# Kernel tuning notes

Measured on AMD Instinct MI355X. Metric: run time of the kernel, lower is better.

## Reference

```python
import math
import jax, jax.numpy as jnp
import numpy as np


def _procrustes_R(H):
    # H: [B, 3, 3]. Rotation R = V @ U^T with reflection fix (det(R) >= 0),
    # matching torch.svd convention (v = V, not V^T).
    u, s, vh = jnp.linalg.svd(H)
    v = jnp.swapaxes(vh, -1, -2)                       # [B,3,3]
    r = jnp.einsum('bij,bkj->bik', v, u)               # V @ U^T
    det = jnp.linalg.det(r)                            # [B]
    sign = jnp.where(det < 0, -1.0, 1.0)               # flip last column of V (reflect = diag(1,1,-1))
    flip = jnp.stack([jnp.ones_like(sign), jnp.ones_like(sign), sign], axis=-1)[:, None, :]
    v = v * flip
    return jnp.einsum('bij,bkj->bik', v, u)


def setup_inputs() -> dict:
    key = jax.random.key(0)
    k1, k2, k3, k4 = jax.random.split(key, 4)
    B, D, N, M = 8, 512, 2048, 2048
    return {
        'src_embedding': jax.random.normal(k1, (B, D, N), dtype=jnp.float32),
        'tgt_embedding': jax.random.normal(k2, (B, D, M), dtype=jnp.float32),
        'src': jax.random.normal(k3, (B, 3, N), dtype=jnp.float32),
        'tgt': jax.random.normal(k4, (B, 3, M), dtype=jnp.float32),
    }


def reference(src_embedding, tgt_embedding, src, tgt):
    d_k = src_embedding.shape[1]
    # attention correspondence: scores[b,n,m]
    scores = jnp.einsum('bdn,bdm->bnm', src_embedding, tgt_embedding) / math.sqrt(d_k)
    scores = jax.nn.softmax(scores, axis=2)
    # soft correspondence of src points in tgt: [B,3,N]
    src_corr = jnp.einsum('bdm,bnm->bdn', tgt, scores)
    src_mean = src.mean(axis=2, keepdims=True)          # [B,3,1]
    src_centered = src - src_mean
    src_corr_centered = src_corr - src_corr.mean(axis=2, keepdims=True)
    H = jnp.einsum('bin,bjn->bij', src_centered, src_corr_centered)  # [B,3,3]
    R = _procrustes_R(H)
    t = jnp.einsum('bij,bjk->bik', -R, src_mean) + tgt.mean(axis=2, keepdims=True)
    return R, t.reshape(src.shape[0], 3)
```

## Files before the change

### kernel.cpp

```cpp
#include <hip/hip_runtime.h>
#include <hip/hip_bf16.h>

#define BQ 8
#define DIM 512
#define NN 2048
#define MM 2048
#define MSPLIT 16

typedef __attribute__((ext_vector_type(8))) short short8;
typedef __attribute__((ext_vector_type(8))) unsigned short ushort8;
typedef __attribute__((ext_vector_type(4))) float floatx4;

#define GLOAD_LDS(gp, lp) \
    __builtin_amdgcn_global_load_lds( \
        (const __attribute__((address_space(1))) void*)(gp), \
        (__attribute__((address_space(3))) void*)(lp), 16, 0, 0)


static __device__ __forceinline__ unsigned short f2bf(float x) {
    __hip_bfloat16 h = __float2bfloat16(x);
    return *(unsigned short*)&h;
}

__global__ __launch_bounds__(256) void transpose_cast_kernel(
    const float* __restrict__ src_emb,
    const float* __restrict__ tgt_emb,
    __hip_bfloat16* __restrict__ Abf,
    __hip_bfloat16* __restrict__ Bbf)
{
    const int n0 = blockIdx.x * 64;
    const int d0 = blockIdx.y * 64;
    const int b  = blockIdx.z & 7;
    const int which = blockIdx.z >> 3;

    const float* in = (which == 0 ? src_emb : tgt_emb) + (size_t)b * DIM * NN;
    __hip_bfloat16* out = (which == 0 ? Abf : Bbf) + (size_t)b * NN * DIM;

    __shared__ float tl[64][65];

    const int t = threadIdx.x;

    {
        const int u = t & 15;
        const int r = t >> 4;
        #pragma unroll
        for (int rr = r; rr < 64; rr += 16) {
            float4 v = *(const float4*)&in[(size_t)(d0 + rr) * NN + n0 + u * 4];
            tl[rr][u * 4 + 0] = v.x;
            tl[rr][u * 4 + 1] = v.y;
            tl[rr][u * 4 + 2] = v.z;
            tl[rr][u * 4 + 3] = v.w;
        }
    }
    __syncthreads();

    {
        const int u = t & 7;
        const int r = t >> 3;
        #pragma unroll
        for (int rn = r; rn < 64; rn += 32) {
            ushort8 o;
            #pragma unroll
            for (int j = 0; j < 8; j++)
                o[j] = f2bf(tl[u * 8 + j][rn]);
            *(ushort8*)&out[(size_t)(n0 + rn) * DIM + d0 + u * 8] = o;
        }
    }
}

__global__ __launch_bounds__(256, 2) void attn_mfma_kernel(
    const __hip_bfloat16* __restrict__ Abf,
    const __hip_bfloat16* __restrict__ Bbf,
    const float* __restrict__ tgt,
    float* __restrict__ part)
{
    const int nt = blockIdx.x;
    const int qt = blockIdx.y;
    const int b  = blockIdx.z;
    const int t  = threadIdx.x;
    const int wave = t >> 6;
    const int lane = t & 63;
    const int lm   = lane & 15;
    const int quad = lane >> 4;
    const int wn   = wave * 32;

    __shared__ short As[128 * 64];
    __shared__ short Bs[128 * 64];

    const __hip_bfloat16* Abase = Abf + ((size_t)(b * NN + nt * 128)) * DIM;
    const int m0 = qt * 128;
    const __hip_bfloat16* Bbase = Bbf + ((size_t)(b * MM + m0)) * DIM;
    const float* Tb = tgt + (size_t)b * 3 * MM;

    const float SCALE = 0.044194173824159216f * 1.4426950408889634f;

    const int r8 = lane >> 3;
    const int c8 = lane & 7;
    const int cc = c8 ^ r8;
    const __hip_bfloat16* gA = Abase + (size_t)(wn + r8) * DIM + cc * 8;
    const __hip_bfloat16* gB = Bbase + (size_t)(wn + r8) * DIM + cc * 8;
    short* lA = &As[wn * 64];
    short* lB = &Bs[wn * 64];

    floatx4 acc[2][8];
    #pragma unroll
    for (int i = 0; i < 2; i++)
        #pragma unroll
        for (int j = 0; j < 8; j++)
            acc[i][j] = (floatx4){0.f, 0.f, 0.f, 0.f};

    #pragma unroll
    for (int kt = 0; kt < 8; kt++) {
        #pragma unroll
        for (int i = 0; i < 4; i++) {
            GLOAD_LDS(gA + kt * 64 + (size_t)i * 8 * DIM, lA + i * 512);
            GLOAD_LDS(gB + kt * 64 + (size_t)i * 8 * DIM, lB + i * 512);
        }
        __syncthreads();

        #pragma unroll
        for (int ks = 0; ks < 2; ks++) {
            const int pc = (((ks * 4 + quad) ^ (lane & 7)) * 8);
            short8 af0 = *(const short8*)&As[(wn +      lm) * 64 + pc];
            short8 af1 = *(const short8*)&As[(wn + 16 + lm) * 64 + pc];
            #pragma unroll
            for (int j = 0; j < 8; j++) {
                short8 bf = *(const short8*)&Bs[(j * 16 + lm) * 64 + pc];
                acc[0][j] = __builtin_amdgcn_mfma_f32_16x16x32_bf16(af0, bf, acc[0][j], 0, 0, 0);
                acc[1][j] = __builtin_amdgcn_mfma_f32_16x16x32_bf16(af1, bf, acc[1][j], 0, 0, 0);
            }
        }
        __syncthreads();
    }

    float v0[8], v1[8], v2[8];
    #pragma unroll
    for (int j = 0; j < 8; j++) {
        int vc = m0 + j * 16 + lm;
        v0[j] = Tb[vc];
        v1[j] = Tb[MM + vc];
        v2[j] = Tb[2 * MM + vc];
    }

    const size_t slot = (size_t)(b * MSPLIT + qt) * NN;
    #pragma unroll
    for (int i = 0; i < 2; i++) {
        float l4[4] = {0,0,0,0};
        float o0[4] = {0,0,0,0};
        float o1[4] = {0,0,0,0};
        float o2[4] = {0,0,0,0};
        #pragma unroll
        for (int j = 0; j < 8; j++) {
            #pragma unroll
            for (int r = 0; r < 4; r++) {
                float e = __builtin_amdgcn_exp2f(acc[i][j][r] * SCALE);
                l4[r] += e;
                o0[r] += e * v0[j];
                o1[r] += e * v1[j];
                o2[r] += e * v2[j];
            }
        }
        #pragma unroll
        for (int m = 1; m <= 8; m <<= 1) {
            #pragma unroll
            for (int r = 0; r < 4; r++) {
                l4[r] += __shfl_xor(l4[r], m);
                o0[r] += __shfl_xor(o0[r], m);
                o1[r] += __shfl_xor(o1[r], m);
                o2[r] += __shfl_xor(o2[r], m);
            }
        }
        if (lm == 0) {
            #pragma unroll
            for (int r = 0; r < 4; r++) {
                int n = nt * 128 + wn + i * 16 + quad * 4 + r;
                ((float4*)part)[slot + n] = make_float4(l4[r], o0[r], o1[r], o2[r]);
            }
        }
    }
}

__global__ __launch_bounds__(128) void reduce1_kernel(
    const float* __restrict__ part,
    const float* __restrict__ src,
    const float* __restrict__ tgt,
    float* __restrict__ red)
{
    const int chunk = blockIdx.x;
    const int b     = blockIdx.y;
    const int t     = threadIdx.x;
    const int n     = chunk * 128 + t;

    const float4* w4 = (const float4*)part;
    const float* S = src + (size_t)b * 3 * NN;
    const float* T = tgt + (size_t)b * 3 * MM;

    float l = 0.f, y0 = 0.f, y1 = 0.f, y2 = 0.f;
    #pragma unroll
    for (int q = 0; q < 16; q++) {
        float4 p = w4[(size_t)(b * 16 + q) * NN + n];
        l += p.x; y0 += p.y; y1 += p.z; y2 += p.w;
    }
    float inv = 1.0f / l;
    float c0 = y0 * inv, c1 = y1 * inv, c2 = y2 * inv;
    float s0 = S[n], s1 = S[NN + n], s2 = S[2 * NN + n];

    float vals[18];
    vals[0] = s0;  vals[1] = s1;  vals[2] = s2;
    vals[3] = c0;  vals[4] = c1;  vals[5] = c2;
    vals[6] = T[n]; vals[7] = T[MM + n]; vals[8] = T[2 * MM + n];
    vals[9]  = s0 * c0; vals[10] = s0 * c1; vals[11] = s0 * c2;
    vals[12] = s1 * c0; vals[13] = s1 * c1; vals[14] = s1 * c2;
    vals[15] = s2 * c0; vals[16] = s2 * c1; vals[17] = s2 * c2;

    #pragma unroll
    for (int m = 1; m <= 32; m <<= 1)
        #pragma unroll
        for (int c = 0; c < 18; c++)
            vals[c] += __shfl_xor(vals[c], m);

    __shared__ float w0[18];
    if (t == 64)
        #pragma unroll
        for (int c = 0; c < 18; c++) w0[c] = vals[c];
    __syncthreads();
    if (t == 0)
        #pragma unroll
        for (int c = 0; c < 18; c++)
            red[(size_t)(b * 16 + chunk) * 18 + c] = vals[c] + w0[c];
}

__global__ __launch_bounds__(64) void procrustes_kernel(
    const float* __restrict__ red,
    float* __restrict__ out)
{
    const int b = blockIdx.x;
    const int t = threadIdx.x;

    __shared__ float res[18];
    if (t < 18) {
        float a = 0.f;
        #pragma unroll
        for (int q = 0; q < 16; q++)
            a += red[(size_t)(b * 16 + q) * 18 + t];
        res[t] = a;
    }
    __syncthreads();

    if (t == 0) {
        const float invN = 1.0f / (float)NN;
        float mus[3], muc[3], mut[3], H[3][3];
        for (int i = 0; i < 3; i++) {
            mus[i] = res[i] * invN;
            muc[i] = res[3 + i] * invN;
            mut[i] = res[6 + i] * invN;
        }
        for (int i = 0; i < 3; i++)
            for (int j = 0; j < 3; j++)
                H[i][j] = res[9 + i * 3 + j] - (float)NN * mus[i] * muc[j];

        float A[3][3];
        for (int i = 0; i < 3; i++)
            for (int j = 0; j < 3; j++)
                A[i][j] = H[0][i] * H[0][j] + H[1][i] * H[1][j] + H[2][i] * H[2][j];

        float V[3][3] = {{1,0,0},{0,1,0},{0,0,1}};
        for (int sweep = 0; sweep < 6; sweep++) {
            for (int pi = 0; pi < 3; pi++) {
                int p = (pi < 2) ? 0 : 1;
                int q = (pi == 0) ? 1 : 2;
                float apq = A[p][q];
                if (fabsf(apq) < 1e-30f) continue;
                float tau = (A[q][q] - A[p][p]) / (2.0f * apq);
                float tt = (tau >= 0.0f) ? 1.0f / (tau + sqrtf(1.0f + tau * tau))
                                         : -1.0f / (-tau + sqrtf(1.0f + tau * tau));
                float c = 1.0f / sqrtf(1.0f + tt * tt);
                float s = tt * c;
                for (int k = 0; k < 3; k++) {
                    float akp = A[k][p], akq = A[k][q];
                    A[k][p] = c * akp - s * akq;
                    A[k][q] = s * akp + c * akq;
                }
                for (int k = 0; k < 3; k++) {
                    float apk = A[p][k], aqk = A[q][k];
                    A[p][k] = c * apk - s * aqk;
                    A[q][k] = s * apk + c * aqk;
                }
                for (int k = 0; k < 3; k++) {
                    float vkp = V[k][p], vkq = V[k][q];
                    V[k][p] = c * vkp - s * vkq;
                    V[k][q] = s * vkp + c * vkq;
                }
            }
        }

        float lam[3] = {A[0][0], A[1][1], A[2][2]};
        int idx[3] = {0, 1, 2};
        for (int a = 0; a < 2; a++)
            for (int bb = 0; bb < 2 - a; bb++)
                if (lam[idx[bb]] < lam[idx[bb + 1]]) { int tmp = idx[bb]; idx[bb] = idx[bb + 1]; idx[bb + 1] = tmp; }

        float Vc[3][3], U[3][3];
        for (int c = 0; c < 3; c++) {
            float sv = sqrtf(fmaxf(lam[idx[c]], 0.0f));
            float isv = 1.0f / fmaxf(sv, 1e-20f);
            for (int r = 0; r < 3; r++) {
                Vc[r][c] = V[r][idx[c]];
                U[r][c] = (H[r][0] * V[0][idx[c]] + H[r][1] * V[1][idx[c]] + H[r][2] * V[2][idx[c]]) * isv;
            }
        }

        {
            float nrm = rsqrtf(U[0][0]*U[0][0] + U[1][0]*U[1][0] + U[2][0]*U[2][0]);
            for (int r = 0; r < 3; r++) U[r][0] *= nrm;
            float d01 = U[0][0]*U[0][1] + U[1][0]*U[1][1] + U[2][0]*U[2][1];
            for (int r = 0; r < 3; r++) U[r][1] -= d01 * U[r][0];
            nrm = rsqrtf(U[0][1]*U[0][1] + U[1][1]*U[1][1] + U[2][1]*U[2][1]);
            for (int r = 0; r < 3; r++) U[r][1] *= nrm;
            float d02 = U[0][0]*U[0][2] + U[1][0]*U[1][2] + U[2][0]*U[2][2];
            float d12 = U[0][1]*U[0][2] + U[1][1]*U[1][2] + U[2][1]*U[2][2];
            for (int r = 0; r < 3; r++) U[r][2] -= d02 * U[r][0] + d12 * U[r][1];
            nrm = rsqrtf(U[0][2]*U[0][2] + U[1][2]*U[1][2] + U[2][2]*U[2][2]);
            for (int r = 0; r < 3; r++) U[r][2] *= nrm;
        }

        float det = H[0][0]*(H[1][1]*H[2][2] - H[1][2]*H[2][1])
                  - H[0][1]*(H[1][0]*H[2][2] - H[1][2]*H[2][0])
                  + H[0][2]*(H[1][0]*H[2][1] - H[1][1]*H[2][0]);
        float sgn = (det < 0.0f) ? -1.0f : 1.0f;

        float R[3][3];
        for (int i = 0; i < 3; i++)
            for (int j = 0; j < 3; j++)
                R[i][j] = Vc[i][0]*U[j][0] + Vc[i][1]*U[j][1] + sgn * Vc[i][2]*U[j][2];

        for (int i = 0; i < 3; i++)
            for (int j = 0; j < 3; j++)
                out[b * 9 + i * 3 + j] = R[i][j];
        for (int i = 0; i < 3; i++)
            out[BQ * 9 + b * 3 + i] = mut[i] - (R[i][0]*mus[0] + R[i][1]*mus[1] + R[i][2]*mus[2]);
    }
}

extern "C" void kernel_launch(void* const* d_in, const int* in_sizes, int n_in,
                              void* d_out, int out_size, void* d_ws, size_t ws_size,
                              hipStream_t stream) {
    const float* src_emb = (const float*)d_in[0];
    const float* tgt_emb = (const float*)d_in[1];
    const float* src     = (const float*)d_in[2];
    const float* tgt     = (const float*)d_in[3];
    float* out = (float*)d_out;

    float* part = (float*)d_ws;
    __hip_bfloat16* Abf = (__hip_bfloat16*)((char*)d_ws + (4 << 20));
    __hip_bfloat16* Bbf = (__hip_bfloat16*)((char*)d_ws + (20 << 20));
    float* red = (float*)((char*)d_ws + (36 << 20));

    dim3 gridT(NN / 64, DIM / 64, 2 * BQ);
    transpose_cast_kernel<<<gridT, 256, 0, stream>>>(src_emb, tgt_emb, Abf, Bbf);

    dim3 gridA(NN / 128, MSPLIT, BQ);
    attn_mfma_kernel<<<gridA, 256, 0, stream>>>(Abf, Bbf, tgt, part);

    dim3 gridR(16, BQ);
    reduce1_kernel<<<gridR, 128, 0, stream>>>(part, src, tgt, red);

    procrustes_kernel<<<BQ, 64, 0, stream>>>(red, out);
}
```

Before: 172.0 us.

## Use 2x2 wave tiling in attention MFMA kernel with LDS partial combine

Result: slower. 176.2 us (+2.5%).

```diff
diff --git a/kernel.cpp b/kernel.cpp
--- a/kernel.cpp
+++ b/kernel.cpp
@@ -82,10 +82,13 @@
     const int lane = t & 63;
     const int lm   = lane & 15;
     const int quad = lane >> 4;
-    const int wn   = wave * 32;
+    const int nh = wave >> 1;
+    const int mh = wave & 1;
+    const int wn = wave * 32;
 
     __shared__ short As[128 * 64];
     __shared__ short Bs[128 * 64];
+    __shared__ float4 sc4[2][128];
 
     const __hip_bfloat16* Abase = Abf + ((size_t)(b * NN + nt * 128)) * DIM;
     const int m0 = qt * 128;
@@ -102,11 +105,11 @@
     short* lA = &As[wn * 64];
     short* lB = &Bs[wn * 64];
 
-    floatx4 acc[2][8];
-    #pragma unroll
-    for (int i = 0; i < 2; i++)
-        #pragma unroll
-        for (int j = 0; j < 8; j++)
+    floatx4 acc[4][4];
+    #pragma unroll
+    for (int i = 0; i < 4; i++)
+        #pragma unroll
+        for (int j = 0; j < 4; j++)
             acc[i][j] = (floatx4){0.f, 0.f, 0.f, 0.f};
 
     #pragma unroll
@@ -120,37 +123,41 @@
 
         #pragma unroll
         for (int ks = 0; ks < 2; ks++) {
-            const int pc = (((ks * 4 + quad) ^ (lane & 7)) * 8);
-            short8 af0 = *(const short8*)&As[(wn +      lm) * 64 + pc];
-            short8 af1 = *(const short8*)&As[(wn + 16 + lm) * 64 + pc];
-            #pragma unroll
-            for (int j = 0; j < 8; j++) {
-                short8 bf = *(const short8*)&Bs[(j * 16 + lm) * 64 + pc];
-                acc[0][j] = __builtin_amdgcn_mfma_f32_16x16x32_bf16(af0, bf, acc[0][j], 0, 0, 0);
-                acc[1][j] = __builtin_amdgcn_mfma_f32_16x16x32_bf16(af1, bf, acc[1][j], 0, 0, 0);
-            }
+            const int pc = (((ks * 4 + quad) ^ (lm & 7)) * 8);
+            short8 af[4], bf[4];
+            #pragma unroll
+            for (int i = 0; i < 4; i++)
+                af[i] = *(const short8*)&As[(nh * 64 + i * 16 + lm) * 64 + pc];
+            #pragma unroll
+            for (int j = 0; j < 4; j++)
+                bf[j] = *(const short8*)&Bs[(mh * 64 + j * 16 + lm) * 64 + pc];
+            #pragma unroll
+            for (int i = 0; i < 4; i++)
+                #pragma unroll
+                for (int j = 0; j < 4; j++)
+                    acc[i][j] = __builtin_amdgcn_mfma_f32_16x16x32_bf16(
+                        af[i], bf[j], acc[i][j], 0, 0, 0);
         }
         __syncthreads();
     }
 
-    float v0[8], v1[8], v2[8];
-    #pragma unroll
-    for (int j = 0; j < 8; j++) {
-        int vc = m0 + j * 16 + lm;
+    float v0[4], v1[4], v2[4];
+    #pragma unroll
+    for (int j = 0; j < 4; j++) {
+        int vc = m0 + mh * 64 + j * 16 + lm;
         v0[j] = Tb[vc];
         v1[j] = Tb[MM + vc];
         v2[j] = Tb[2 * MM + vc];
     }
 
-    const size_t slot = (size_t)(b * MSPLIT + qt) * NN;
-    #pragma unroll
-    for (int i = 0; i < 2; i++) {
+    #pragma unroll
+    for (int i = 0; i < 4; i++) {
         float l4[4] = {0,0,0,0};
         float o0[4] = {0,0,0,0};
         float o1[4] = {0,0,0,0};
         float o2[4] = {0,0,0,0};
         #pragma unroll
-        for (int j = 0; j < 8; j++) {
+        for (int j = 0; j < 4; j++) {
             #pragma unroll
             for (int r = 0; r < 4; r++) {
                 float e = __builtin_amdgcn_exp2f(acc[i][j][r] * SCALE);
@@ -172,11 +179,17 @@
         }
         if (lm == 0) {
             #pragma unroll
-            for (int r = 0; r < 4; r++) {
-                int n = nt * 128 + wn + i * 16 + quad * 4 + r;
-                ((float4*)part)[slot + n] = make_float4(l4[r], o0[r], o1[r], o2[r]);
-            }
-        }
+            for (int r = 0; r < 4; r++)
+                sc4[mh][nh * 64 + i * 16 + quad * 4 + r] =
+                    make_float4(l4[r], o0[r], o1[r], o2[r]);
+        }
+    }
+    __syncthreads();
+
+    if (t < 128) {
+        float4 a = sc4[0][t], c = sc4[1][t];
+        ((float4*)part)[(size_t)(b * MSPLIT + qt) * NN + nt * 128 + t] =
+            make_float4(a.x + c.x, a.y + c.y, a.z + c.z, a.w + c.w);
     }
 }
 
```
